# Kernel optimization log

Hardware: AMD Instinct MI355X
Metric: run time of the kernel (lower is better)

The kernel has to match this reference:

```python
import jax, jax.numpy as jnp
import numpy as np
from jax import lax

N = 100000      # nodes
E = 1600000     # edges
F_IN = 128      # nfeat
F_OUT = 32      # nhid


def _l2norm(v, eps=1e-12):
    return v / jnp.maximum(jnp.linalg.norm(v), eps)


def setup_inputs() -> dict:
    key = jax.random.key(0)
    k1, k2, k3, k4, k5 = jax.random.split(key, 5)
    x = jax.random.normal(k1, (N, F_IN), dtype=jnp.float32)
    edge_index = jax.random.randint(k2, (2, E), 0, N, dtype=jnp.int64)
    W = jax.random.normal(k3, (F_OUT, F_IN), dtype=jnp.float32) * (1.0 / np.sqrt(F_IN))
    bias = jax.random.normal(k4, (F_OUT,), dtype=jnp.float32) * 0.01
    prelu_a = jnp.full((1,), 0.25, dtype=jnp.float32)  # PReLU default init
    u_sn = jax.random.normal(k5, (F_OUT,), dtype=jnp.float32)
    return {"x": x, "edge_index": edge_index, "W": W, "bias": bias,
            "prelu_a": prelu_a, "u_sn": u_sn}


def _spectral_norm_weight(W, u):
    # one power iteration (torch default), u/v treated as buffers (no grad)
    v = lax.stop_gradient(_l2norm(W.T @ u))
    u2 = lax.stop_gradient(_l2norm(W @ v))
    sigma = jnp.dot(u2, W @ v)
    return W / sigma


def reference(x, edge_index, W, bias, prelu_a, u_sn):
    W_sn = _spectral_norm_weight(W, u_sn)
    # linear transform first (PyG GCNConv): [N, F_OUT]
    xw = x @ W_sn.T
    # add self loops
    loop = jnp.arange(N, dtype=edge_index.dtype)
    row = jnp.concatenate([edge_index[0], loop])  # source
    col = jnp.concatenate([edge_index[1], loop])  # target
    # symmetric normalization deg^{-1/2} A deg^{-1/2}, deg over targets
    deg = jax.ops.segment_sum(jnp.ones_like(col, dtype=xw.dtype), col, num_segments=N)
    dis = jnp.where(deg > 0, lax.rsqrt(deg), 0.0)
    norm = dis[row] * dis[col]                    # [E+N]
    # gather-scale-scatter aggregation
    msgs = xw[row] * norm[:, None]                # [E+N, F_OUT]
    out = jax.ops.segment_sum(msgs, col, num_segments=N)
    out = out + bias
    # PReLU with single shared slope
    a = prelu_a[0]
    return jnp.where(out >= 0, out, a * out)
```

## Files before the change

### kernel.cpp

```cpp
#include <hip/hip_runtime.h>
#include <hip/hip_fp16.h>

#define F_IN 128
#define F_OUT 32
#define BSH 8
#define BMSK 255

__global__ __launch_bounds__(256) void k1h(
    const float* __restrict__ x, const float* __restrict__ W,
    const float* __restrict__ u, const int* __restrict__ ei,
    __half* __restrict__ xwh, int* __restrict__ M,
    int Nn, int E_, int NB, int P) {
    __shared__ float xs[128 * 65];
    __shared__ float wt[128 * 32];
    __shared__ int   smi[512];
    __shared__ float sv[F_IN];
    __shared__ float sr[F_IN];
    __shared__ float ssc;
    int t = threadIdx.x;
    int p = blockIdx.x;

    for (int b = t; b < NB; b += 256) smi[b] = 0;
    __syncthreads();
    int epb = (E_ + P - 1) / P;
    int e0 = p * epb, e1 = min(e0 + epb, E_);
    const int* col = ei + E_;
    for (int e = e0 + t; e < e1; e += 256)
        atomicAdd(&smi[col[e] >> BSH], 1);
    __syncthreads();
    for (int b = t; b < NB; b += 256) M[(size_t)p * NB + b] = smi[b];

    if (t < F_IN) {
        float a = 0.f;
        for (int i = 0; i < F_OUT; ++i) a += W[i * F_IN + t] * u[i];
        sv[t] = a; sr[t] = a * a;
    }
    __syncthreads();
    for (int o = 64; o > 0; o >>= 1) {
        if (t < o) sr[t] += sr[t + o];
        __syncthreads();
    }
    if (t == 0) ssc = 1.0f / fmaxf(sqrtf(sr[0]), 1e-12f);
    __syncthreads();
    if (t < F_IN) sv[t] *= ssc;
    __syncthreads();
    if (t < F_OUT) {
        float a = 0.f;
        for (int j = 0; j < F_IN; ++j) a += W[t * F_IN + j] * sv[j];
        sr[t] = a * a;
    }
    __syncthreads();
    for (int o = 16; o > 0; o >>= 1) {
        if (t < o) sr[t] += sr[t + o];
        __syncthreads();
    }
    if (t == 0) ssc = 1.0f / fmaxf(sqrtf(sr[0]), 1e-30f);
    __syncthreads();
    float is = ssc;

    int rbase = p * 128;
    {
        int f = t >> 3;
        int kb = 16 * (t & 7);
        const float4* wrow = (const float4*)(W + (size_t)f * F_IN + kb);
#pragma unroll
        for (int j = 0; j < 4; ++j) {
            float4 w = wrow[j];
            int k = kb + 4 * j;
            wt[(k + 0) * 32 + f] = w.x * is;
            wt[(k + 1) * 32 + f] = w.y * is;
            wt[(k + 2) * 32 + f] = w.z * is;
            wt[(k + 3) * 32 + f] = w.w * is;
        }
    }

    int r0 = (t >> 3) * 4;
    int f0 = (t & 7) * 4;
    float4 acc0 = {0, 0, 0, 0}, acc1 = {0, 0, 0, 0};
    float4 acc2 = {0, 0, 0, 0}, acc3 = {0, 0, 0, 0};
    const float4* wt4 = (const float4*)wt;
    int fq = f0 >> 2;

    for (int kc = 0; kc < 2; ++kc) {
        __syncthreads();
        {
            int rr = t >> 4;
            int k0 = 4 * (t & 15);
#pragma unroll
            for (int pi = 0; pi < 8; ++pi) {
                int r = pi * 16 + rr;
                int grow = rbase + r;
                if (grow >= Nn) grow = Nn - 1;
                float4 v = *(const float4*)(x + (size_t)grow * F_IN + kc * 64 + k0);
                xs[r * 65 + k0 + 0] = v.x;
                xs[r * 65 + k0 + 1] = v.y;
                xs[r * 65 + k0 + 2] = v.z;
                xs[r * 65 + k0 + 3] = v.w;
            }
        }
        __syncthreads();
#pragma unroll 4
        for (int kk = 0; kk < 64; ++kk) {
            int k = kc * 64 + kk;
            float4 w = wt4[k * 8 + fq];
            float x0 = xs[(r0 + 0) * 65 + kk];
            float x1 = xs[(r0 + 1) * 65 + kk];
            float x2 = xs[(r0 + 2) * 65 + kk];
            float x3 = xs[(r0 + 3) * 65 + kk];
            acc0.x += x0 * w.x; acc0.y += x0 * w.y; acc0.z += x0 * w.z; acc0.w += x0 * w.w;
            acc1.x += x1 * w.x; acc1.y += x1 * w.y; acc1.z += x1 * w.z; acc1.w += x1 * w.w;
            acc2.x += x2 * w.x; acc2.y += x2 * w.y; acc2.z += x2 * w.z; acc2.w += x2 * w.w;
            acc3.x += x3 * w.x; acc3.y += x3 * w.y; acc3.z += x3 * w.z; acc3.w += x3 * w.w;
        }
    }
    int g0 = rbase + r0;
#pragma unroll
    for (int q = 0; q < 4; ++q) {
        int g = g0 + q;
        if (g < Nn) {
            float4 a = (q == 0) ? acc0 : (q == 1) ? acc1 : (q == 2) ? acc2 : acc3;
            ushort4 s;
            s.x = __half_as_ushort(__float2half(a.x));
            s.y = __half_as_ushort(__float2half(a.y));
            s.z = __half_as_ushort(__float2half(a.z));
            s.w = __half_as_ushort(__float2half(a.w));
            *(ushort4*)(xwh + (size_t)g * F_OUT + f0) = s;
        }
    }
}

__global__ __launch_bounds__(256) void k_scanA(int* __restrict__ M,
                                               int* __restrict__ total,
                                               int NB, int P) {
    __shared__ int sd[256];
    int b = blockIdx.x, t = threadIdx.x;
    int C = (P + 255) >> 8;
    int vals[8];
    int run = 0;
#pragma unroll 4
    for (int j = 0; j < C; ++j) {
        int p = t * C + j;
        int v = (p < P) ? M[(size_t)p * NB + b] : 0;
        vals[j] = run;
        run += v;
    }
    int tsum = run;
    sd[t] = tsum;
    __syncthreads();
    for (int o = 1; o < 256; o <<= 1) {
        int u = (t >= o) ? sd[t - o] : 0;
        __syncthreads();
        sd[t] += u;
        __syncthreads();
    }
    int cb = sd[t] - tsum;
#pragma unroll 4
    for (int j = 0; j < C; ++j) {
        int p = t * C + j;
        if (p < P) M[(size_t)p * NB + b] = cb + vals[j];
    }
    if (t == 255) total[b] = sd[255];
}

__global__ __launch_bounds__(256) void k_scat1(
    const int* __restrict__ ei, const int* __restrict__ M,
    const int* __restrict__ total, int* __restrict__ base,
    unsigned* __restrict__ staging, int E_, int NB, int P) {
    __shared__ int scur[512];
    __shared__ int sd[256];
    int p = blockIdx.x, t = threadIdx.x;
    int C = (NB + 255) >> 8;
    int vals[2];
    int run = 0;
#pragma unroll
    for (int j = 0; j < 2; ++j) {
        int b = t * C + j;
        int v = (j < C && b < NB) ? total[b] : 0;
        vals[j] = run;
        run += v;
    }
    int tsum = run;
    sd[t] = tsum;
    __syncthreads();
    for (int o = 1; o < 256; o <<= 1) {
        int u = (t >= o) ? sd[t - o] : 0;
        __syncthreads();
        sd[t] += u;
        __syncthreads();
    }
    int cb = sd[t] - tsum;
#pragma unroll
    for (int j = 0; j < 2; ++j) {
        int b = t * C + j;
        if (j < C && b < NB) {
            int sb = cb + vals[j];
            scur[b] = sb + M[(size_t)p * NB + b];
            if (p == 0) base[b] = sb;
        }
    }
    if (p == 0 && t == 255) base[NB] = sd[255];
    __syncthreads();
    int epb = (E_ + P - 1) / P;
    int e0 = p * epb, e1 = min(e0 + epb, E_);
    const int* col = ei + E_;
    for (int e = e0 + t; e < e1; e += 256) {
        int c = col[e];
        int r = ei[e];
        int pos = atomicAdd(&scur[c >> BSH], 1);
        staging[pos] = ((unsigned)r << BSH) | (unsigned)(c & BMSK);
    }
}

__global__ __launch_bounds__(256) void k_sort2(
    const unsigned* __restrict__ staging, const int* __restrict__ base,
    int* __restrict__ esr, float* __restrict__ dis,
    int* __restrict__ cursor, int Nn, int E_, int NB) {
    __shared__ int hist[256];
    __shared__ int sd[256];
    __shared__ int lcur[256];
    int b = blockIdx.x, t = threadIdx.x;
    int nb0 = b << BSH;
    int nc = min(256, Nn - nb0);
    hist[t] = 0;
    __syncthreads();
    int s0 = base[b], s1 = base[b + 1];
    for (int j = s0 + t; j < s1; j += 256)
        atomicAdd(&hist[staging[j] & BMSK], 1);
    __syncthreads();
    int h = hist[t];
    if (t < nc) dis[nb0 + t] = rsqrtf((float)h + 1.0f);
    sd[t] = h;
    __syncthreads();
    for (int o = 1; o < 256; o <<= 1) {
        int u = (t >= o) ? sd[t - o] : 0;
        __syncthreads();
        sd[t] += u;
        __syncthreads();
    }
    int excl = sd[t] - h;
    if (t < nc) cursor[nb0 + t] = s0 + excl;
    if (b == NB - 1 && t == 0) cursor[Nn] = E_;
    lcur[t] = s0 + excl;
    __syncthreads();
    for (int j = s0 + t; j < s1; j += 256) {
        unsigned v = staging[j];
        int pp = atomicAdd(&lcur[v & BMSK], 1);
        esr[pp] = (int)(v >> BSH);
    }
}

__global__ __launch_bounds__(256) void k_gather(
    const int* __restrict__ esr, const int* __restrict__ cursor,
    const __half* __restrict__ xwh, const float* __restrict__ dis,
    const float* __restrict__ bias, const float* __restrict__ pa,
    float* __restrict__ out, int Nn) {
    int t = threadIdx.x;
    int node = blockIdx.x * 16 + (t >> 4);
    if (node >= Nn) return;
    int f2 = t & 15;
    int start = cursor[node], end = cursor[node + 1];
    float accx = 0.f, accy = 0.f;
    for (int j0 = start; j0 < end; j0 += 16) {
        int idx = j0 + f2;
        int rf = (idx < end) ? esr[idx] : 0;
        int m = end - j0;
        if (m > 16) m = 16;
        int i = 0;
        for (; i + 4 <= m; i += 4) {
            int r0 = __shfl(rf, i + 0, 16);
            int r1 = __shfl(rf, i + 1, 16);
            int r2 = __shfl(rf, i + 2, 16);
            int r3 = __shfl(rf, i + 3, 16);
            float d0 = dis[r0], d1 = dis[r1], d2 = dis[r2], d3 = dis[r3];
            float2 a0 = __half22float2(*((const __half2*)(xwh + (size_t)r0 * F_OUT) + f2));
            float2 a1 = __half22float2(*((const __half2*)(xwh + (size_t)r1 * F_OUT) + f2));
            float2 a2 = __half22float2(*((const __half2*)(xwh + (size_t)r2 * F_OUT) + f2));
            float2 a3 = __half22float2(*((const __half2*)(xwh + (size_t)r3 * F_OUT) + f2));
            accx += a0.x * d0 + a1.x * d1 + a2.x * d2 + a3.x * d3;
            accy += a0.y * d0 + a1.y * d1 + a2.y * d2 + a3.y * d3;
        }
        for (; i < m; ++i) {
            int r = __shfl(rf, i, 16);
            float d = dis[r];
            float2 a = __half22float2(*((const __half2*)(xwh + (size_t)r * F_OUT) + f2));
            accx += a.x * d;
            accy += a.y * d;
        }
    }
    float dc = dis[node];
    float2 self = __half22float2(*((const __half2*)(xwh + (size_t)node * F_OUT) + f2));
    float2 bi = *((const float2*)bias + f2);
    float a = pa[0];
    float vx = (accx + self.x * dc) * dc + bi.x;
    float vy = (accy + self.y * dc) * dc + bi.y;
    float2 o;
    o.x = (vx >= 0.f) ? vx : a * vx;
    o.y = (vy >= 0.f) ? vy : a * vy;
    *((float2*)(out + (size_t)node * F_OUT) + f2) = o;
}

__global__ void k0_specnorm(const float* __restrict__ W, const float* __restrict__ u,
                            float* __restrict__ Wsc) {
    __shared__ float v[F_IN];
    __shared__ float red[F_IN];
    __shared__ float scal;
    int t = threadIdx.x;
    float acc = 0.f;
    for (int i = 0; i < F_OUT; ++i) acc += W[i * F_IN + t] * u[i];
    v[t] = acc; red[t] = acc * acc;
    __syncthreads();
    if (t == 0) {
        float s = 0.f;
        for (int i = 0; i < F_IN; ++i) s += red[i];
        scal = 1.0f / fmaxf(sqrtf(s), 1e-12f);
    }
    __syncthreads();
    v[t] *= scal;
    __syncthreads();
    if (t < F_OUT) {
        float a2 = 0.f;
        for (int j = 0; j < F_IN; ++j) a2 += W[t * F_IN + j] * v[j];
        red[t] = a2 * a2;
    }
    __syncthreads();
    if (t == 0) {
        float s = 0.f;
        for (int i = 0; i < F_OUT; ++i) s += red[i];
        scal = 1.0f / fmaxf(sqrtf(s), 1e-30f);
    }
    __syncthreads();
    float is = scal;
    for (int i = 0; i < F_OUT; ++i)
        Wsc[i * F_IN + t] = W[i * F_IN + t] * is;
}

__global__ void k1_xw_f32(const float* __restrict__ x, const float* __restrict__ Wsc,
                          const float* __restrict__ dis, float* __restrict__ xw, int Nn) {
    int id = blockIdx.x * blockDim.x + threadIdx.x;
    if (id >= Nn * F_OUT) return;
    int r = id >> 5, f = id & 31;
    const float4* x4 = (const float4*)(x + (size_t)r * F_IN);
    const float4* w4 = (const float4*)(Wsc + (size_t)f * F_IN);
    float acc = 0.f;
#pragma unroll
    for (int k = 0; k < F_IN / 4; ++k) {
        float4 a = x4[k];
        float4 b = w4[k];
        acc += a.x * b.x + a.y * b.y + a.z * b.z + a.w * b.w;
    }
    xw[id] = acc * dis[r];
}

__global__ void k2_deg(const int* __restrict__ col, int* __restrict__ cnt, int E_) {
    int e = blockIdx.x * blockDim.x + threadIdx.x;
    if (e < E_) atomicAdd(&cnt[col[e]], 1);
}

__global__ void k3_dis(const int* __restrict__ cnt, float* __restrict__ dis, int Nn) {
    int i = blockIdx.x * blockDim.x + threadIdx.x;
    if (i < Nn) dis[i] = rsqrtf((float)cnt[i] + 1.0f);
}

__global__ void k4_scatter(const int* __restrict__ ei, const float* __restrict__ xws,
                           const float* __restrict__ dis, float* __restrict__ out, int E_) {
    int id = blockIdx.x * blockDim.x + threadIdx.x;
    if (id >= E_ * F_OUT) return;
    int e = id >> 5, f = id & 31;
    int r = ei[e];
    int c = ei[E_ + e];
    atomicAdd(&out[(size_t)c * F_OUT + f], xws[(size_t)r * F_OUT + f] * dis[c]);
}

__global__ void k5_epi(const float* __restrict__ xws, const float* __restrict__ dis,
                       const float* __restrict__ bias, const float* __restrict__ pa,
                       float* __restrict__ out, int Nn) {
    int id = blockIdx.x * blockDim.x + threadIdx.x;
    if (id >= Nn * F_OUT) return;
    int i = id >> 5, f = id & 31;
    float d = dis[i];
    float v = out[id] + xws[id] * d + bias[f];
    float a = pa[0];
    out[id] = (v >= 0.f) ? v : a * v;
}

extern "C" void kernel_launch(void* const* d_in, const int* in_sizes, int n_in,
                              void* d_out, int out_size, void* d_ws, size_t ws_size,
                              hipStream_t stream) {
    const float* x    = (const float*)d_in[0];
    const int*   ei   = (const int*)d_in[1];
    const float* W    = (const float*)d_in[2];
    const float* bias = (const float*)d_in[3];
    const float* pa   = (const float*)d_in[4];
    const float* u    = (const float*)d_in[5];

    int Nn = in_sizes[0] / F_IN;
    int E_ = in_sizes[1] / 2;
    float* out = (float*)d_out;

    int NB = (Nn + BMSK) >> BSH;
    int P  = (Nn + 127) / 128;

    size_t o = 0;
    __half*   xwh     = (__half*)d_ws;       o += (size_t)Nn * (F_OUT / 2);
    float*    dis     = (float*)d_ws + o;    o += Nn;
    int*      cursor  = (int*)d_ws + o;      o += Nn + 1;
    int*      M       = (int*)d_ws + o;      o += (size_t)P * NB;
    int*      total   = (int*)d_ws + o;      o += NB;
    int*      base    = (int*)d_ws + o;      o += NB + 1;
    unsigned* staging = (unsigned*)d_ws + o; o += E_;
    int*      esr     = (int*)d_ws + o;      o += E_;
    bool big_ws = (ws_size >= o * sizeof(float)) && (NB <= 512) && (P <= 2048);

    if (big_ws) {
        k1h<<<P, 256, 0, stream>>>(x, W, u, ei, xwh, M, Nn, E_, NB, P);
        k_scanA<<<NB, 256, 0, stream>>>(M, total, NB, P);
        k_scat1<<<P, 256, 0, stream>>>(ei, M, total, base, staging, E_, NB, P);
        k_sort2<<<NB, 256, 0, stream>>>(staging, base, esr, dis, cursor, Nn, E_, NB);
        k_gather<<<(Nn + 15) / 16, 256, 0, stream>>>(esr, cursor, xwh, dis, bias, pa, out, Nn);
    } else {
        size_t o2 = 0;
        float* xw2  = (float*)d_ws;       o2 += (size_t)Nn * F_OUT;
        float* Wsc2 = (float*)d_ws + o2;  o2 += F_OUT * F_IN;
        float* dis2 = (float*)d_ws + o2;  o2 += Nn;
        int*   deg2 = (int*)d_ws + o2;    o2 += Nn;
        hipMemsetAsync(deg2, 0, (size_t)Nn * sizeof(int), stream);
        hipMemsetAsync(d_out, 0, (size_t)Nn * F_OUT * sizeof(float), stream);
        k0_specnorm<<<1, 128, 0, stream>>>(W, u, Wsc2);
        k2_deg<<<(E_ + 255) / 256, 256, 0, stream>>>(ei + E_, deg2, E_);
        k3_dis<<<(Nn + 255) / 256, 256, 0, stream>>>(deg2, dis2, Nn);
        int nT1 = Nn * F_OUT;
        k1_xw_f32<<<(nT1 + 255) / 256, 256, 0, stream>>>(x, Wsc2, dis2, xw2, Nn);
        int nT4 = E_ * F_OUT;
        k4_scatter<<<(nT4 + 255) / 256, 256, 0, stream>>>(ei, xw2, dis2, out, E_);
        k5_epi<<<(nT1 + 255) / 256, 256, 0, stream>>>(xw2, dis2, bias, pa, out, Nn);
    }
}
```

Baseline: 189.3 us.

## Prescale xw by source deg^-1/2 and split histogram from GEMM kernel

Edge histogramming moves out of the GEMM kernel into its own kernel with a fixed 256 partitions. The bucket width shrinks to 128 nodes, and the partition-count matrix is transposed so each scan block reads it contiguously. The GEMM now runs after the sort, once dis is known, and stores xw already multiplied by the source node's deg^-1/2. This removes the random per-edge dis loads and multiplies from the gather loop. In exchange there is one extra kernel launch, and the GEMM can no longer overlap with the histogram work.

```diff
diff --git a/kernel.cpp b/kernel.cpp
--- a/kernel.cpp
+++ b/kernel.cpp
@@ -3,32 +3,137 @@
 
 #define F_IN 128
 #define F_OUT 32
-#define BSH 8
-#define BMSK 255
-
-__global__ __launch_bounds__(256) void k1h(
+#define PBLK 256
+#define BSH 7
+#define BMSK 127
+#define MAXB 1024
+
+__global__ __launch_bounds__(256) void k_hist(const int* __restrict__ col,
+                                              int* __restrict__ M, int E_, int NB) {
+    __shared__ int h[MAXB];
+    int p = blockIdx.x, t = threadIdx.x;
+    for (int b = t; b < NB; b += 256) h[b] = 0;
+    __syncthreads();
+    int epb = (E_ + PBLK - 1) / PBLK;
+    int e0 = p * epb, e1 = min(e0 + epb, E_);
+    for (int e = e0 + t; e < e1; e += 256)
+        atomicAdd(&h[col[e] >> BSH], 1);
+    __syncthreads();
+    for (int b = t; b < NB; b += 256) M[(size_t)b * PBLK + p] = h[b];
+}
+
+__global__ __launch_bounds__(256) void k_scanA(int* __restrict__ M,
+                                               int* __restrict__ total, int NB) {
+    __shared__ int sd[256];
+    int b = blockIdx.x, t = threadIdx.x;
+    int v = M[(size_t)b * PBLK + t];
+    sd[t] = v;
+    __syncthreads();
+    for (int o = 1; o < 256; o <<= 1) {
+        int u = (t >= o) ? sd[t - o] : 0;
+        __syncthreads();
+        sd[t] += u;
+        __syncthreads();
+    }
+    M[(size_t)b * PBLK + t] = sd[t] - v;
+    if (t == 255) total[b] = sd[255];
+}
+
+__global__ __launch_bounds__(256) void k_scat1(
+    const int* __restrict__ ei, const int* __restrict__ M,
+    const int* __restrict__ total, int* __restrict__ base,
+    unsigned* __restrict__ staging, int E_, int NB) {
+    __shared__ int scur[MAXB];
+    __shared__ int sd[256];
+    int p = blockIdx.x, t = threadIdx.x;
+    int C = (NB + 255) >> 8;
+    int vals[4];
+    int run = 0;
+    for (int j = 0; j < C; ++j) {
+        int b = t * C + j;
+        int v = (b < NB) ? total[b] : 0;
+        vals[j] = run;
+        run += v;
+    }
+    int tsum = run;
+    sd[t] = tsum;
+    __syncthreads();
+    for (int o = 1; o < 256; o <<= 1) {
+        int u = (t >= o) ? sd[t - o] : 0;
+        __syncthreads();
+        sd[t] += u;
+        __syncthreads();
+    }
+    int cb = sd[t] - tsum;
+    for (int j = 0; j < C; ++j) {
+        int b = t * C + j;
+        if (b < NB) {
+            int sb = cb + vals[j];
+            scur[b] = sb + M[(size_t)b * PBLK + p];
+            if (p == 0) base[b] = sb;
+        }
+    }
+    if (p == 0 && t == 255) base[NB] = sd[255];
+    __syncthreads();
+    int epb = (E_ + PBLK - 1) / PBLK;
+    int e0 = p * epb, e1 = min(e0 + epb, E_);
+    const int* col = ei + E_;
+    for (int e = e0 + t; e < e1; e += 256) {
+        int c = col[e];
+        int r = ei[e];
+        int pos = atomicAdd(&scur[c >> BSH], 1);
+        staging[pos] = ((unsigned)r << BSH) | (unsigned)(c & BMSK);
+    }
+}
+
+__global__ __launch_bounds__(256) void k_sort2(
+    const unsigned* __restrict__ staging, const int* __restrict__ base,
+    int* __restrict__ esr, float* __restrict__ dis,
+    int* __restrict__ cursor, int Nn, int E_, int NB) {
+    __shared__ int hist[256];
+    __shared__ int sd[256];
+    __shared__ int lcur[256];
+    int b = blockIdx.x, t = threadIdx.x;
+    int nb0 = b << BSH;
+    int nc = min(1 << BSH, Nn - nb0);
+    hist[t] = 0;
+    __syncthreads();
+    int s0 = base[b], s1 = base[b + 1];
+    for (int j = s0 + t; j < s1; j += 256)
+        atomicAdd(&hist[staging[j] & BMSK], 1);
+    __syncthreads();
+    int h = hist[t];
+    if (t < nc) dis[nb0 + t] = rsqrtf((float)h + 1.0f);
+    sd[t] = h;
+    __syncthreads();
+    for (int o = 1; o < 256; o <<= 1) {
+        int u = (t >= o) ? sd[t - o] : 0;
+        __syncthreads();
+        sd[t] += u;
+        __syncthreads();
+    }
+    int excl = sd[t] - h;
+    if (t < nc) cursor[nb0 + t] = s0 + excl;
+    if (b == NB - 1 && t == 0) cursor[Nn] = E_;
+    lcur[t] = s0 + excl;
+    __syncthreads();
+    for (int j = s0 + t; j < s1; j += 256) {
+        unsigned v = staging[j];
+        int pp = atomicAdd(&lcur[v & BMSK], 1);
+        esr[pp] = (int)(v >> BSH);
+    }
+}
+
+__global__ __launch_bounds__(256) void k1_xw(
     const float* __restrict__ x, const float* __restrict__ W,
-    const float* __restrict__ u, const int* __restrict__ ei,
-    __half* __restrict__ xwh, int* __restrict__ M,
-    int Nn, int E_, int NB, int P) {
+    const float* __restrict__ u, const float* __restrict__ dis,
+    __half* __restrict__ xwh, int Nn) {
     __shared__ float xs[128 * 65];
     __shared__ float wt[128 * 32];
-    __shared__ int   smi[512];
     __shared__ float sv[F_IN];
     __shared__ float sr[F_IN];
     __shared__ float ssc;
     int t = threadIdx.x;
-    int p = blockIdx.x;
-
-    for (int b = t; b < NB; b += 256) smi[b] = 0;
-    __syncthreads();
-    int epb = (E_ + P - 1) / P;
-    int e0 = p * epb, e1 = min(e0 + epb, E_);
-    const int* col = ei + E_;
-    for (int e = e0 + t; e < e1; e += 256)
-        atomicAdd(&smi[col[e] >> BSH], 1);
-    __syncthreads();
-    for (int b = t; b < NB; b += 256) M[(size_t)p * NB + b] = smi[b];
 
     if (t < F_IN) {
         float a = 0.f;
@@ -58,7 +163,7 @@
     __syncthreads();
     float is = ssc;
 
-    int rbase = p * 128;
+    int rbase = blockIdx.x * 128;
     {
         int f = t >> 3;
         int kb = 16 * (t & 7);
@@ -118,140 +223,21 @@
     for (int q = 0; q < 4; ++q) {
         int g = g0 + q;
         if (g < Nn) {
+            float d = dis[g];
             float4 a = (q == 0) ? acc0 : (q == 1) ? acc1 : (q == 2) ? acc2 : acc3;
             ushort4 s;
-            s.x = __half_as_ushort(__float2half(a.x));
-            s.y = __half_as_ushort(__float2half(a.y));
-            s.z = __half_as_ushort(__float2half(a.z));
-            s.w = __half_as_ushort(__float2half(a.w));
+            s.x = __half_as_ushort(__float2half(a.x * d));
+            s.y = __half_as_ushort(__float2half(a.y * d));
+            s.z = __half_as_ushort(__float2half(a.z * d));
+            s.w = __half_as_ushort(__float2half(a.w * d));
             *(ushort4*)(xwh + (size_t)g * F_OUT + f0) = s;
         }
-    }
-}
-
-__global__ __launch_bounds__(256) void k_scanA(int* __restrict__ M,
-                                               int* __restrict__ total,
-                                               int NB, int P) {
-    __shared__ int sd[256];
-    int b = blockIdx.x, t = threadIdx.x;
-    int C = (P + 255) >> 8;
-    int vals[8];
-    int run = 0;
-#pragma unroll 4
-    for (int j = 0; j < C; ++j) {
-        int p = t * C + j;
-        int v = (p < P) ? M[(size_t)p * NB + b] : 0;
-        vals[j] = run;
-        run += v;
-    }
-    int tsum = run;
-    sd[t] = tsum;
-    __syncthreads();
-    for (int o = 1; o < 256; o <<= 1) {
-        int u = (t >= o) ? sd[t - o] : 0;
-        __syncthreads();
-        sd[t] += u;
-        __syncthreads();
-    }
-    int cb = sd[t] - tsum;
-#pragma unroll 4
-    for (int j = 0; j < C; ++j) {
-        int p = t * C + j;
-        if (p < P) M[(size_t)p * NB + b] = cb + vals[j];
-    }
-    if (t == 255) total[b] = sd[255];
-}
-
-__global__ __launch_bounds__(256) void k_scat1(
-    const int* __restrict__ ei, const int* __restrict__ M,
-    const int* __restrict__ total, int* __restrict__ base,
-    unsigned* __restrict__ staging, int E_, int NB, int P) {
-    __shared__ int scur[512];
-    __shared__ int sd[256];
-    int p = blockIdx.x, t = threadIdx.x;
-    int C = (NB + 255) >> 8;
-    int vals[2];
-    int run = 0;
-#pragma unroll
-    for (int j = 0; j < 2; ++j) {
-        int b = t * C + j;
-        int v = (j < C && b < NB) ? total[b] : 0;
-        vals[j] = run;
-        run += v;
-    }
-    int tsum = run;
-    sd[t] = tsum;
-    __syncthreads();
-    for (int o = 1; o < 256; o <<= 1) {
-        int u = (t >= o) ? sd[t - o] : 0;
-        __syncthreads();
-        sd[t] += u;
-        __syncthreads();
-    }
-    int cb = sd[t] - tsum;
-#pragma unroll
-    for (int j = 0; j < 2; ++j) {
-        int b = t * C + j;
-        if (j < C && b < NB) {
-            int sb = cb + vals[j];
-            scur[b] = sb + M[(size_t)p * NB + b];
-            if (p == 0) base[b] = sb;
-        }
-    }
-    if (p == 0 && t == 255) base[NB] = sd[255];
-    __syncthreads();
-    int epb = (E_ + P - 1) / P;
-    int e0 = p * epb, e1 = min(e0 + epb, E_);
-    const int* col = ei + E_;
-    for (int e = e0 + t; e < e1; e += 256) {
-        int c = col[e];
-        int r = ei[e];
-        int pos = atomicAdd(&scur[c >> BSH], 1);
-        staging[pos] = ((unsigned)r << BSH) | (unsigned)(c & BMSK);
-    }
-}
-
-__global__ __launch_bounds__(256) void k_sort2(
-    const unsigned* __restrict__ staging, const int* __restrict__ base,
-    int* __restrict__ esr, float* __restrict__ dis,
-    int* __restrict__ cursor, int Nn, int E_, int NB) {
-    __shared__ int hist[256];
-    __shared__ int sd[256];
-    __shared__ int lcur[256];
-    int b = blockIdx.x, t = threadIdx.x;
-    int nb0 = b << BSH;
-    int nc = min(256, Nn - nb0);
-    hist[t] = 0;
-    __syncthreads();
-    int s0 = base[b], s1 = base[b + 1];
-    for (int j = s0 + t; j < s1; j += 256)
-        atomicAdd(&hist[staging[j] & BMSK], 1);
-    __syncthreads();
-    int h = hist[t];
-    if (t < nc) dis[nb0 + t] = rsqrtf((float)h + 1.0f);
-    sd[t] = h;
-    __syncthreads();
-    for (int o = 1; o < 256; o <<= 1) {
-        int u = (t >= o) ? sd[t - o] : 0;
-        __syncthreads();
-        sd[t] += u;
-        __syncthreads();
-    }
-    int excl = sd[t] - h;
-    if (t < nc) cursor[nb0 + t] = s0 + excl;
-    if (b == NB - 1 && t == 0) cursor[Nn] = E_;
-    lcur[t] = s0 + excl;
-    __syncthreads();
-    for (int j = s0 + t; j < s1; j += 256) {
-        unsigned v = staging[j];
-        int pp = atomicAdd(&lcur[v & BMSK], 1);
-        esr[pp] = (int)(v >> BSH);
     }
 }
 
 __global__ __launch_bounds__(256) void k_gather(
     const int* __restrict__ esr, const int* __restrict__ cursor,
-    const __half* __restrict__ xwh, const float* __restrict__ dis,
+    const __half* __restrict__ xws, const float* __restrict__ dis,
     const float* __restrict__ bias, const float* __restrict__ pa,
     float* __restrict__ out, int Nn) {
     int t = threadIdx.x;
@@ -271,28 +257,26 @@
             int r1 = __shfl(rf, i + 1, 16);
             int r2 = __shfl(rf, i + 2, 16);
             int r3 = __shfl(rf, i + 3, 16);
-            float d0 = dis[r0], d1 = dis[r1], d2 = dis[r2], d3 = dis[r3];
-            float2 a0 = __half22float2(*((const __half2*)(xwh + (size_t)r0 * F_OUT) + f2));
-            float2 a1 = __half22float2(*((const __half2*)(xwh + (size_t)r1 * F_OUT) + f2));
-            float2 a2 = __half22float2(*((const __half2*)(xwh + (size_t)r2 * F_OUT) + f2));
-            float2 a3 = __half22float2(*((const __half2*)(xwh + (size_t)r3 * F_OUT) + f2));
-            accx += a0.x * d0 + a1.x * d1 + a2.x * d2 + a3.x * d3;
-            accy += a0.y * d0 + a1.y * d1 + a2.y * d2 + a3.y * d3;
+            float2 a0 = __half22float2(*((const __half2*)(xws + (size_t)r0 * F_OUT) + f2));
+            float2 a1 = __half22float2(*((const __half2*)(xws + (size_t)r1 * F_OUT) + f2));
+            float2 a2 = __half22float2(*((const __half2*)(xws + (size_t)r2 * F_OUT) + f2));
+            float2 a3 = __half22float2(*((const __half2*)(xws + (size_t)r3 * F_OUT) + f2));
+            accx += a0.x + a1.x + a2.x + a3.x;
+            accy += a0.y + a1.y + a2.y + a3.y;
         }
         for (; i < m; ++i) {
             int r = __shfl(rf, i, 16);
-            float d = dis[r];
-            float2 a = __half22float2(*((const __half2*)(xwh + (size_t)r * F_OUT) + f2));
-            accx += a.x * d;
-            accy += a.y * d;
+            float2 a = __half22float2(*((const __half2*)(xws + (size_t)r * F_OUT) + f2));
+            accx += a.x;
+            accy += a.y;
         }
     }
     float dc = dis[node];
-    float2 self = __half22float2(*((const __half2*)(xwh + (size_t)node * F_OUT) + f2));
+    float2 self = __half22float2(*((const __half2*)(xws + (size_t)node * F_OUT) + f2));
     float2 bi = *((const float2*)bias + f2);
     float a = pa[0];
-    float vx = (accx + self.x * dc) * dc + bi.x;
-    float vy = (accy + self.y * dc) * dc + bi.y;
+    float vx = (accx + self.x) * dc + bi.x;
+    float vy = (accy + self.y) * dc + bi.y;
     float2 o;
     o.x = (vx >= 0.f) ? vx : a * vx;
     o.y = (vy >= 0.f) ? vy : a * vy;
@@ -398,24 +382,24 @@
     float* out = (float*)d_out;
 
     int NB = (Nn + BMSK) >> BSH;
-    int P  = (Nn + 127) / 128;
 
     size_t o = 0;
     __half*   xwh     = (__half*)d_ws;       o += (size_t)Nn * (F_OUT / 2);
     float*    dis     = (float*)d_ws + o;    o += Nn;
     int*      cursor  = (int*)d_ws + o;      o += Nn + 1;
-    int*      M       = (int*)d_ws + o;      o += (size_t)P * NB;
+    int*      M       = (int*)d_ws + o;      o += (size_t)NB * PBLK;
     int*      total   = (int*)d_ws + o;      o += NB;
     int*      base    = (int*)d_ws + o;      o += NB + 1;
     unsigned* staging = (unsigned*)d_ws + o; o += E_;
     int*      esr     = (int*)d_ws + o;      o += E_;
-    bool big_ws = (ws_size >= o * sizeof(float)) && (NB <= 512) && (P <= 2048);
+    bool big_ws = (ws_size >= o * sizeof(float)) && (NB <= MAXB);
 
     if (big_ws) {
-        k1h<<<P, 256, 0, stream>>>(x, W, u, ei, xwh, M, Nn, E_, NB, P);
-        k_scanA<<<NB, 256, 0, stream>>>(M, total, NB, P);
-        k_scat1<<<P, 256, 0, stream>>>(ei, M, total, base, staging, E_, NB, P);
+        k_hist<<<PBLK, 256, 0, stream>>>(ei + E_, M, E_, NB);
+        k_scanA<<<NB, 256, 0, stream>>>(M, total, NB);
+        k_scat1<<<PBLK, 256, 0, stream>>>(ei, M, total, base, staging, E_, NB);
         k_sort2<<<NB, 256, 0, stream>>>(staging, base, esr, dis, cursor, Nn, E_, NB);
+        k1_xw<<<(Nn + 127) / 128, 256, 0, stream>>>(x, W, u, dis, xwh, Nn);
         k_gather<<<(Nn + 15) / 16, 256, 0, stream>>>(esr, cursor, xwh, dis, bias, pa, out, Nn);
     } else {
         size_t o2 = 0;
```

New measurement: 190.8 us. No clear change (+0.8%).
